# Performance work log

Hardware: AMD Instinct MI355X
Metric: run time of the kernel (lower is better)

The kernel has to match this reference:

```python
import jax, jax.numpy as jnp
import numpy as np

N = 200_000   # nodes per type
F_IN = 64     # input features per node type
H = 8         # hidden_channels (heads=1)
E = 3_000_000 # edges per edge type


def setup_inputs() -> dict:
    key = jax.random.key(0)
    ks = jax.random.split(key, 40)
    d = {}
    d['x_ind'] = jax.random.normal(ks[0], (N, F_IN), jnp.float32)
    d['x_org'] = jax.random.normal(ks[1], (N, F_IN), jnp.float32)
    d['x_ext'] = jax.random.normal(ks[2], (N, F_IN), jnp.float32)
    d['ei_ind_org'] = jax.random.randint(ks[3], (2, E), 0, N, jnp.int32)
    d['ei_org_ind'] = jax.random.randint(ks[4], (2, E), 0, N, jnp.int32)
    d['ei_ext_ind'] = jax.random.randint(ks[5], (2, E), 0, N, jnp.int32)
    d['ei_ext_org'] = jax.random.randint(ks[6], (2, E), 0, N, jnp.int32)
    s_in = 1.0 / np.sqrt(F_IN)
    # per-node-type projections (Linear(F_IN, H) with bias)
    for i, nt in enumerate(('ind', 'org', 'ext')):
        d[f'W_{nt}'] = jax.random.normal(ks[7 + i], (F_IN, H), jnp.float32) * s_in
        d[f'b_{nt}'] = jnp.zeros((H,), jnp.float32)
    # per-edge-type GAT attention vectors (heads=1, so shape [H])
    for i, et in enumerate(('ind_org', 'org_ind', 'ext_ind', 'ext_org')):
        d[f'att_src_{et}'] = jax.random.normal(ks[10 + 2 * i], (H,), jnp.float32) * (1.0 / np.sqrt(H))
        d[f'att_dst_{et}'] = jax.random.normal(ks[11 + 2 * i], (H,), jnp.float32) * (1.0 / np.sqrt(H))
    # semantic attention: k_lin(H->H) + query q
    d['k_W'] = jax.random.normal(ks[20], (H, H), jnp.float32) * (1.0 / np.sqrt(H))
    d['k_b'] = jnp.zeros((H,), jnp.float32)
    d['q'] = jax.random.normal(ks[21], (H,), jnp.float32)
    # prediction heads
    d['lin_ind_W'] = jax.random.normal(ks[22], (H, 1), jnp.float32) * (1.0 / np.sqrt(H))
    d['lin_ind_b'] = jnp.zeros((1,), jnp.float32)
    d['lin_org_W'] = jax.random.normal(ks[23], (H, 1), jnp.float32) * (1.0 / np.sqrt(H))
    d['lin_org_b'] = jnp.zeros((1,), jnp.float32)
    return d


def _gat_edge(h_src, h_dst, a_src, a_dst, ei):
    """Per-edge-type GAT message passing with segment softmax over dst."""
    row, col = ei[0], ei[1]
    alpha_s = h_src @ a_src  # [N]
    alpha_d = h_dst @ a_dst  # [N]
    alpha = jax.nn.leaky_relu(alpha_s[row] + alpha_d[col], 0.2)  # [E]
    m = jax.lax.stop_gradient(jax.ops.segment_max(alpha, col, num_segments=N))
    m = jnp.where(jnp.isfinite(m), m, 0.0)
    ex = jnp.exp(alpha - m[col])
    den = jax.ops.segment_sum(ex, col, num_segments=N) + 1e-16
    w = ex / den[col]  # [E]
    out = jax.ops.segment_sum(h_src[row] * w[:, None], col, num_segments=N)  # [N,H]
    return jax.nn.relu(out)


def _group(outs, q, k_W, k_b):
    """Semantic-level attention over metapath embeddings."""
    o = jnp.stack(outs)  # [M, N, H]
    score = (jnp.tanh(o @ k_W + k_b) @ q).mean(axis=1)  # [M]
    attn = jax.nn.softmax(score)
    return jnp.einsum('m,mnf->nf', attn, o)


def reference(x_ind, x_org, x_ext,
              ei_ind_org, ei_org_ind, ei_ext_ind, ei_ext_org,
              W_ind, b_ind, W_org, b_org, W_ext, b_ext,
              att_src_ind_org, att_dst_ind_org,
              att_src_org_ind, att_dst_org_ind,
              att_src_ext_ind, att_dst_ext_ind,
              att_src_ext_org, att_dst_ext_org,
              k_W, k_b, q,
              lin_ind_W, lin_ind_b, lin_org_W, lin_org_b):
    h_ind = x_ind @ W_ind + b_ind  # [N,H]
    h_org = x_org @ W_org + b_org
    h_ext = x_ext @ W_ext + b_ext
    # metapaths into 'ind'
    outs_ind = [
        _gat_edge(h_org, h_ind, att_src_org_ind, att_dst_org_ind, ei_org_ind),
        _gat_edge(h_ext, h_ind, att_src_ext_ind, att_dst_ext_ind, ei_ext_ind),
    ]
    # metapaths into 'org'
    outs_org = [
        _gat_edge(h_ind, h_org, att_src_ind_org, att_dst_ind_org, ei_ind_org),
        _gat_edge(h_ext, h_org, att_src_ext_org, att_dst_ext_org, ei_ext_org),
    ]
    z_ind = _group(outs_ind, q, k_W, k_b)  # [N,H]
    z_org = _group(outs_org, q, k_W, k_b)
    pred_ind = jax.nn.sigmoid(z_ind @ lin_ind_W + lin_ind_b)[:, 0]
    pred_org = jax.nn.sigmoid(z_org @ lin_org_W + lin_org_b)[:, 0]
    return (pred_ind, pred_org)
```

## Files before the change

kernel.cpp:

```cpp
#include <hip/hip_runtime.h>
#include <hip/hip_fp16.h>

#define HH 8
#define FIN 64
#define CHUNK 8192
#define NPB 1024
#define NPB_SHIFT 10
#define MAXNB 256
#define SUBCH 16384
#define RSH 18
#define RMASK 0x3FFFFu

typedef float vfloat4 __attribute__((ext_vector_type(4)));

__device__ __forceinline__ float b2f(unsigned short u) {
  union { unsigned int i; float f; } x;
  x.i = ((unsigned int)u) << 16;
  return x.f;
}

__device__ __forceinline__ float lrelu(float x) { return x > 0.f ? x : 0.2f * x; }

__device__ __forceinline__ float ld(const void* p, int i, int isf) {
  return isf ? ((const float*)p)[i] : b2f(((const unsigned short*)p)[i]);
}

__device__ __forceinline__ float tanhf_fast(float x) {
  float xc = fminf(fmaxf(x, -15.f), 15.f);
  float e = __expf(2.f * xc);
  return 1.f - 2.f / (e + 1.f);
}

struct MP {
  const int* ei;
  const float* as;
  const float* ad;
  const __half* hs;
  float* den;
  float* out;
  unsigned* sorted;
  int* gcur;
  int E;
  int nchunks;
  int rcap;
};
struct MP4 { MP m[4]; };

struct PJ {
  const void* x; const void* W; const void* b; __half* h16;
  const void* a0; float* s0;
  const void* a1; float* s1;
  const void* a2; float* s2;
};
struct PJ3 { PJ p[3]; };

struct SC { const float *o0, *d0, *o1, *d1; float* score; };
struct SC2 { SC g[2]; };
struct PR { const float *o0, *d0, *o1, *d1; const float* score;
            const void* linW; const void* linb; float* outp; };
struct PR2 { PR g[2]; };

__global__ void __launch_bounds__(1024)
setup_kernel(const unsigned short* __restrict__ x, int* __restrict__ flag,
             float* __restrict__ score_all, int* __restrict__ gcur, int rcap) {
  __shared__ int tot;
  int t = threadIdx.x;
  gcur[t] = (t & 255) * rcap;
  if (t < 4) score_all[t] = 0.f;
  if (t == 0) tot = 0;
  __syncthreads();
  int cnt = 0;
  for (int i = t; i < 2048; i += 1024) {
    int e = (x[i] >> 7) & 0xFF;
    if (e >= 0x90) cnt++;
  }
  if (cnt) atomicAdd(&tot, cnt);
  __syncthreads();
  if (t == 0) flag[0] = (tot >= 8) ? 1 : 0;
}

__global__ void __launch_bounds__(256)
proj_kernel(PJ3 pj, int N, const int* __restrict__ flag) {
  const PJ P = pj.p[blockIdx.y];
  __shared__ float Wl[FIN][HH];
  __shared__ float bl[HH];
  __shared__ float al[3][HH];
  int isf = flag[0];
  int t = threadIdx.x;
  for (int i = t; i < FIN * HH; i += blockDim.x) Wl[i >> 3][i & 7] = ld(P.W, i, isf);
  if (t < HH) {
    bl[t] = ld(P.b, t, isf);
    al[0][t] = P.a0 ? ld(P.a0, t, isf) : 0.f;
    al[1][t] = P.a1 ? ld(P.a1, t, isf) : 0.f;
    al[2][t] = P.a2 ? ld(P.a2, t, isf) : 0.f;
  }
  __syncthreads();
  int n = blockIdx.x * blockDim.x + t;
  if (n >= N) return;
  float acc[HH];
#pragma unroll
  for (int j = 0; j < HH; ++j) acc[j] = bl[j];
  if (isf) {
    const float4* xr = (const float4*)((const float*)P.x + (size_t)n * FIN);
#pragma unroll
    for (int v = 0; v < FIN / 4; ++v) {
      float4 p = xr[v];
      float f4[4] = {p.x, p.y, p.z, p.w};
#pragma unroll
      for (int k = 0; k < 4; ++k) {
        int f = v * 4 + k;
#pragma unroll
        for (int j = 0; j < HH; ++j) acc[j] += f4[k] * Wl[f][j];
      }
    }
  } else {
    const uint4* xr = (const uint4*)((const unsigned short*)P.x + (size_t)n * FIN);
#pragma unroll
    for (int v = 0; v < FIN / 8; ++v) {
      uint4 p = xr[v];
      unsigned int w[4] = {p.x, p.y, p.z, p.w};
#pragma unroll
      for (int k = 0; k < 4; ++k) {
        float f0 = __uint_as_float(w[k] << 16);
        float f1 = __uint_as_float(w[k] & 0xFFFF0000u);
        int f = v * 8 + k * 2;
#pragma unroll
        for (int j = 0; j < HH; ++j) acc[j] += f0 * Wl[f][j];
#pragma unroll
        for (int j = 0; j < HH; ++j) acc[j] += f1 * Wl[f + 1][j];
      }
    }
  }
  union { __half h[8]; uint4 u; } pk;
#pragma unroll
  for (int j = 0; j < HH; ++j) pk.h[j] = __float2half(acc[j]);
  *(uint4*)(P.h16 + (size_t)n * HH) = pk.u;
  float d0 = 0.f, d1 = 0.f, d2 = 0.f;
#pragma unroll
  for (int j = 0; j < HH; ++j) {
    d0 += acc[j] * al[0][j];
    d1 += acc[j] * al[1][j];
    d2 += acc[j] * al[2][j];
  }
  if (P.s0) P.s0[n] = d0;
  if (P.s1) P.s1[n] = d1;
  if (P.s2) P.s2[n] = d2;
}

__global__ void __launch_bounds__(512)
partA(MP4 a4, int mp_base, int NB) {
  const MP a = a4.m[mp_base + blockIdx.y];
  int k = blockIdx.x;
  if (k >= a.nchunks) return;
  __shared__ unsigned buf[CHUNK];
  __shared__ int cnt[MAXNB];
  __shared__ int cur[MAXNB];
  __shared__ int off[MAXNB];
  __shared__ int posA[MAXNB];
  int t = threadIdx.x;
  int E = a.E;
  int base = k * CHUNK;
  int len = E - base; if (len > CHUNK) len = CHUNK;
  if (t < MAXNB) cnt[t] = 0;
  __syncthreads();
  int rr[16], cc[16];
  if (len == CHUNK && ((E & 3) == 0)) {
    const int4* eir = (const int4*)(a.ei + base);
    const int4* eic = (const int4*)(a.ei + E + base);
#pragma unroll
    for (int j = 0; j < 4; ++j) {
      int4 r4 = eir[j * 512 + t];
      int4 c4 = eic[j * 512 + t];
      rr[j * 4 + 0] = r4.x; cc[j * 4 + 0] = c4.x;
      rr[j * 4 + 1] = r4.y; cc[j * 4 + 1] = c4.y;
      rr[j * 4 + 2] = r4.z; cc[j * 4 + 2] = c4.z;
      rr[j * 4 + 3] = r4.w; cc[j * 4 + 3] = c4.w;
    }
  } else {
#pragma unroll
    for (int j = 0; j < 16; ++j) {
      int idx = j * 512 + t;
      rr[j] = -1;
      if (idx < len) { rr[j] = a.ei[base + idx]; cc[j] = a.ei[E + base + idx]; }
    }
  }
#pragma unroll
  for (int j = 0; j < 16; ++j)
    if (rr[j] >= 0) atomicAdd(&cnt[cc[j] >> NPB_SHIFT], 1);
  __syncthreads();
  if (t < 64) {
    int b0 = t * 4;
    int c0 = cnt[b0], c1 = cnt[b0 + 1], c2 = cnt[b0 + 2], c3 = cnt[b0 + 3];
    int s = c0 + c1 + c2 + c3;
    int inc = s;
#pragma unroll
    for (int d = 1; d < 64; d <<= 1) {
      int v = __shfl_up(inc, d, 64);
      if (t >= d) inc += v;
    }
    int run = inc - s;
    off[b0] = run;          cur[b0] = run;
    off[b0 + 1] = run + c0; cur[b0 + 1] = run + c0;
    off[b0 + 2] = run + c0 + c1; cur[b0 + 2] = run + c0 + c1;
    off[b0 + 3] = run + c0 + c1 + c2; cur[b0 + 3] = run + c0 + c1 + c2;
    posA[b0]     = c0 ? atomicAdd(&a.gcur[b0], c0) : 0;
    posA[b0 + 1] = c1 ? atomicAdd(&a.gcur[b0 + 1], c1) : 0;
    posA[b0 + 2] = c2 ? atomicAdd(&a.gcur[b0 + 2], c2) : 0;
    posA[b0 + 3] = c3 ? atomicAdd(&a.gcur[b0 + 3], c3) : 0;
  }
  __syncthreads();
#pragma unroll
  for (int j = 0; j < 16; ++j) {
    if (rr[j] >= 0) {
      int bb = cc[j] >> NPB_SHIFT;
      int p = atomicAdd(&cur[bb], 1);
      buf[p] = ((unsigned)(cc[j] & (NPB - 1)) << RSH) | (unsigned)rr[j];
    }
  }
  __syncthreads();
  int wv = t >> 6, ln = t & 63;
  for (int s = wv; s < NB; s += 8) {
    int cn = cnt[s];
    if (cn == 0) continue;
    int c0 = off[s];
    int gb = posA[s];
    int lim = (s + 1) * a.rcap;
    int mx = lim - gb; if (mx < 0) mx = 0;
    if (cn > mx) cn = mx;
    for (int j = ln; j < cn; j += 64)
      __builtin_nontemporal_store(buf[c0 + j], &a.sorted[(size_t)gb + j]);
  }
}

__global__ void __launch_bounds__(1024)
partB(MP4 a4, int mp_base, int NB, int N, int fused) {
  int mp, b;
  if (fused) {
    int blk = blockIdx.x;
    int xcd = blk & 7;
    mp = xcd >> 1;
    b = ((blk >> 3) << 1) + (xcd & 1);
    if (b >= NB) return;
  } else {
    mp = mp_base;
    b = blockIdx.x;
  }
  const MP a = a4.m[mp];
  __shared__ unsigned key2[SUBCH];
  __shared__ int cnt2[NPB];
  __shared__ int o2[NPB];
  __shared__ int cur2[NPB];
  int t = threadIdx.x;
  int s0i = b * a.rcap;
  int cnt = a.gcur[b] - s0i;
  if (cnt < 0) cnt = 0;
  if (cnt > a.rcap) cnt = a.rcap;
  const unsigned* run = a.sorted + (size_t)s0i;
  int basen = b << NPB_SHIFT;
  int n0 = basen + t;
  float ad0 = (n0 < N) ? a.ad[n0] : 0.f;
  const float* asp = a.as;
  const __half* hs = a.hs;

  float acc0[HH];
#pragma unroll
  for (int f = 0; f < HH; ++f) acc0[f] = 0.f;
  float dn0 = 0.f;

  for (int c0 = 0; c0 < cnt; c0 += SUBCH) {
    int m = cnt - c0; if (m > SUBCH) m = SUBCH;
    cnt2[t] = 0;
    __syncthreads();
    for (int idx = t; idx < m; idx += 1024) {
      unsigned v = __builtin_nontemporal_load(run + c0 + idx);
      atomicAdd(&cnt2[v >> RSH], 1);
    }
    __syncthreads();
    if (t < 64) {
      int c[16];
      int s = 0;
#pragma unroll
      for (int j = 0; j < 16; ++j) { c[j] = cnt2[t * 16 + j]; s += c[j]; }
      int inc = s;
#pragma unroll
      for (int d = 1; d < 64; d <<= 1) {
        int v = __shfl_up(inc, d, 64);
        if (t >= d) inc += v;
      }
      int run2 = inc - s;
#pragma unroll
      for (int j = 0; j < 16; ++j) {
        o2[t * 16 + j] = run2;
        cur2[t * 16 + j] = run2;
        run2 += c[j];
      }
    }
    __syncthreads();
    for (int idx = t; idx < m; idx += 1024) {
      unsigned v = __builtin_nontemporal_load(run + c0 + idx);
      int p = atomicAdd(&cur2[v >> RSH], 1);
      key2[p] = v;
    }
    __syncthreads();
    int j = o2[t], e = cur2[t];
    while (j < e) {
      int cn = e - j; if (cn > 4) cn = 4;
      int r[4];
      float av[4];
      uint4 hv[4];
#pragma unroll
      for (int u = 0; u < 4; ++u) r[u] = (u < cn) ? (int)(key2[j + u] & RMASK) : -1;
#pragma unroll
      for (int u = 0; u < 4; ++u)
        if (r[u] >= 0) { av[u] = asp[r[u]]; hv[u] = *(const uint4*)(hs + (size_t)r[u] * HH); }
#pragma unroll
      for (int u = 0; u < 4; ++u) {
        if (r[u] >= 0) {
          float w = __expf(lrelu(av[u] + ad0));
          dn0 += w;
          union { uint4 q; __half h[8]; } H; H.q = hv[u];
#pragma unroll
          for (int f = 0; f < HH; ++f) acc0[f] += w * __half2float(H.h[f]);
        }
      }
      j += cn;
    }
    if (c0 + SUBCH < cnt) __syncthreads();
  }
  if (n0 < N) {
    vfloat4* po = (vfloat4*)(a.out + (size_t)n0 * HH);
    vfloat4 v0 = {acc0[0], acc0[1], acc0[2], acc0[3]};
    vfloat4 v1 = {acc0[4], acc0[5], acc0[6], acc0[7]};
    __builtin_nontemporal_store(v0, po + 0);
    __builtin_nontemporal_store(v1, po + 1);
    __builtin_nontemporal_store(dn0, &a.den[n0]);
  }
}

__global__ void __launch_bounds__(256)
score_kernel(SC2 sc, int N,
             const void* __restrict__ kW, const void* __restrict__ kb,
             const void* __restrict__ qv, const int* __restrict__ flag) {
  const SC S = sc.g[blockIdx.y];
  __shared__ float kWl[HH][HH];
  __shared__ float kbl[HH], ql[HH];
  __shared__ float r0[4], r1[4];
  int isf = flag[0];
  int t = threadIdx.x;
  if (t < HH * HH) kWl[t >> 3][t & 7] = ld(kW, t, isf);
  if (t < HH) { kbl[t] = ld(kb, t, isf); ql[t] = ld(qv, t, isf); }
  __syncthreads();
  int n = blockIdx.x * blockDim.x + t;
  float s0 = 0.f, s1 = 0.f;
  if (n < N) {
    const float* p0 = S.o0 + (size_t)n * HH;
    const float* p1 = S.o1 + (size_t)n * HH;
    float i0 = 1.f / (S.d0[n] + 1e-16f);
    float i1 = 1.f / (S.d1[n] + 1e-16f);
    float v0[HH], v1[HH];
#pragma unroll
    for (int j = 0; j < HH; ++j) { v0[j] = fmaxf(p0[j] * i0, 0.f); v1[j] = fmaxf(p1[j] * i1, 0.f); }
#pragma unroll
    for (int j = 0; j < HH; ++j) {
      float t0 = kbl[j], t1 = kbl[j];
#pragma unroll
      for (int i = 0; i < HH; ++i) { t0 += v0[i] * kWl[i][j]; t1 += v1[i] * kWl[i][j]; }
      s0 += tanhf_fast(t0) * ql[j];
      s1 += tanhf_fast(t1) * ql[j];
    }
  }
#pragma unroll
  for (int d = 32; d > 0; d >>= 1) {
    s0 += __shfl_down(s0, d, 64);
    s1 += __shfl_down(s1, d, 64);
  }
  int wv = t >> 6, ln = t & 63;
  if (ln == 0) { r0[wv] = s0; r1[wv] = s1; }
  __syncthreads();
  if (t == 0) {
    atomicAdd(&S.score[0], r0[0] + r0[1] + r0[2] + r0[3]);
    atomicAdd(&S.score[1], r1[0] + r1[1] + r1[2] + r1[3]);
  }
}

__global__ void __launch_bounds__(256)
pred_kernel(PR2 pr, int N, const int* __restrict__ flag) {
  const PR P = pr.g[blockIdx.y];
  int isf = flag[0];
  int n = blockIdx.x * blockDim.x + threadIdx.x;
  if (n >= N) return;
  float s0 = P.score[0] / (float)N, s1 = P.score[1] / (float)N;
  float mx = fmaxf(s0, s1);
  float e0 = __expf(s0 - mx), e1 = __expf(s1 - mx);
  float inv = 1.f / (e0 + e1);
  float a0 = e0 * inv, a1 = e1 * inv;
  const float* p0 = P.o0 + (size_t)n * HH;
  const float* p1 = P.o1 + (size_t)n * HH;
  float i0 = 1.f / (P.d0[n] + 1e-16f);
  float i1 = 1.f / (P.d1[n] + 1e-16f);
  float acc = ld(P.linb, 0, isf);
#pragma unroll
  for (int j = 0; j < HH; ++j) {
    float z = a0 * fmaxf(p0[j] * i0, 0.f) + a1 * fmaxf(p1[j] * i1, 0.f);
    acc += z * ld(P.linW, j, isf);
  }
  P.outp[n] = 1.f / (1.f + __expf(-acc));
}

extern "C" void kernel_launch(void* const* d_in, const int* in_sizes, int n_in,
                              void* d_out, int out_size, void* d_ws, size_t ws_size,
                              hipStream_t stream) {
  const int N = in_sizes[0] / FIN;

  const void* x_ind = d_in[0];
  const void* x_org = d_in[1];
  const void* x_ext = d_in[2];
  const int* ei_io = (const int*)d_in[3];  int E_io = in_sizes[3] / 2;
  const int* ei_oi = (const int*)d_in[4];  int E_oi = in_sizes[4] / 2;
  const int* ei_ei = (const int*)d_in[5];  int E_ei = in_sizes[5] / 2;
  const int* ei_eo = (const int*)d_in[6];  int E_eo = in_sizes[6] / 2;
  const void* W_ind = d_in[7];
  const void* b_ind = d_in[8];
  const void* W_org = d_in[9];
  const void* b_org = d_in[10];
  const void* W_ext = d_in[11];
  const void* b_ext = d_in[12];
  const void* att_src_io = d_in[13];
  const void* att_dst_io = d_in[14];
  const void* att_src_oi = d_in[15];
  const void* att_dst_oi = d_in[16];
  const void* att_src_ei = d_in[17];
  const void* att_dst_ei = d_in[18];
  const void* att_src_eo = d_in[19];
  const void* att_dst_eo = d_in[20];
  const void* k_W = d_in[21];
  const void* k_b = d_in[22];
  const void* qv  = d_in[23];
  const void* lin_ind_W = d_in[24];
  const void* lin_ind_b = d_in[25];
  const void* lin_org_W = d_in[26];
  const void* lin_org_b = d_in[27];

  float* out_f = (float*)d_out;

  int E_max = E_io;
  if (E_oi > E_max) E_max = E_oi;
  if (E_ei > E_max) E_max = E_ei;
  if (E_eo > E_max) E_max = E_eo;

  const int NB = (N + NPB - 1) >> NPB_SHIFT;
  const int nchunks_max = (E_max + CHUNK - 1) / CHUNK;
  const int rcap = (int)(((long long)E_max / NB) * 115 / 100) + 128;

  float* ws = (float*)d_ws;
  size_t off = 0;
  __half* h16_ind = (__half*)(ws + off); off += (size_t)N * HH / 2;
  __half* h16_org = (__half*)(ws + off); off += (size_t)N * HH / 2;
  __half* h16_ext = (__half*)(ws + off); off += (size_t)N * HH / 2;
  float* as_io = ws + off; off += N;
  float* ad_oi = ws + off; off += N;
  float* ad_ei = ws + off; off += N;
  float* as_oi = ws + off; off += N;
  float* ad_io = ws + off; off += N;
  float* ad_eo = ws + off; off += N;
  float* as_ei = ws + off; off += N;
  float* as_eo = ws + off; off += N;
  float* den_all = ws + off; off += (size_t)4 * N;
  float* out_all = ws + off; off += (size_t)4 * N * HH;
  float* score_all = ws + off; off += 4;
  int* flag = (int*)(ws + off); off += 1;
  off = (off + 1) & ~(size_t)1;
  int* gcur0 = (int*)(ws + off); off += 4 * 256;

  size_t sort_f = (size_t)NB * rcap;
  bool big = (off + 4 * sort_f) * sizeof(float) <= ws_size;
  int slots = big ? 4 : 1;
  unsigned* sorted0 = (unsigned*)(ws + off); off += (size_t)slots * sort_f;

  const int BS = 256;
  const int nb_node = (N + BS - 1) / BS;

  setup_kernel<<<1, 1024, 0, stream>>>((const unsigned short*)x_ind, flag, score_all, gcur0, rcap);

  PJ3 pj;
  pj.p[0] = PJ{x_ind, W_ind, b_ind, h16_ind, att_src_io, as_io, att_dst_oi, ad_oi, att_dst_ei, ad_ei};
  pj.p[1] = PJ{x_org, W_org, b_org, h16_org, att_src_oi, as_oi, att_dst_io, ad_io, att_dst_eo, ad_eo};
  pj.p[2] = PJ{x_ext, W_ext, b_ext, h16_ext, att_src_ei, as_ei, att_src_eo, as_eo, nullptr, nullptr};
  proj_kernel<<<dim3(nb_node, 3), BS, 0, stream>>>(pj, N, flag);

  const int* eis[4]       = {ei_oi, ei_ei, ei_io, ei_eo};
  int        Es[4]        = {E_oi, E_ei, E_io, E_eo};
  const float* ass[4]     = {as_oi, as_ei, as_io, as_eo};
  const float* ads[4]     = {ad_oi, ad_ei, ad_io, ad_eo};
  const __half* hsrcs[4]  = {h16_org, h16_ext, h16_ind, h16_ext};

  MP4 a4;
  for (int mp = 0; mp < 4; ++mp) {
    MP& a = a4.m[mp];
    a.ei = eis[mp];
    a.as = ass[mp];
    a.ad = ads[mp];
    a.hs = hsrcs[mp];
    a.den = den_all + (size_t)mp * N;
    a.out = out_all + (size_t)mp * N * HH;
    a.sorted = sorted0 + (size_t)(big ? mp : 0) * sort_f;
    a.gcur = gcur0 + mp * 256;
    a.E = Es[mp];
    a.nchunks = (Es[mp] + CHUNK - 1) / CHUNK;
    a.rcap = rcap;
  }

  if (big) {
    partA<<<dim3(nchunks_max, 4), 512, 0, stream>>>(a4, 0, NB);
    int nblkB = 8 * ((NB + 1) >> 1);
    partB<<<dim3(nblkB, 1), 1024, 0, stream>>>(a4, 0, NB, N, 1);
  } else {
    for (int mp = 0; mp < 4; ++mp) {
      partA<<<dim3(a4.m[mp].nchunks, 1), 512, 0, stream>>>(a4, mp, NB);
      partB<<<dim3(NB, 1), 1024, 0, stream>>>(a4, mp, NB, N, 0);
    }
  }

  float* o_ind0 = out_all + (size_t)0 * N * HH;
  float* o_ind1 = out_all + (size_t)1 * N * HH;
  float* o_org0 = out_all + (size_t)2 * N * HH;
  float* o_org1 = out_all + (size_t)3 * N * HH;
  float* d_ind0 = den_all + (size_t)0 * N;
  float* d_ind1 = den_all + (size_t)1 * N;
  float* d_org0 = den_all + (size_t)2 * N;
  float* d_org1 = den_all + (size_t)3 * N;

  SC2 sc;
  sc.g[0] = SC{o_ind0, d_ind0, o_ind1, d_ind1, score_all};
  sc.g[1] = SC{o_org0, d_org0, o_org1, d_org1, score_all + 2};
  score_kernel<<<dim3(nb_node, 2), BS, 0, stream>>>(sc, N, k_W, k_b, qv, flag);

  PR2 pr;
  pr.g[0] = PR{o_ind0, d_ind0, o_ind1, d_ind1, score_all, lin_ind_W, lin_ind_b, out_f};
  pr.g[1] = PR{o_org0, d_org0, o_org1, d_org1, score_all + 2, lin_org_W, lin_org_b, out_f + N};
  pred_kernel<<<dim3(nb_node, 2), BS, 0, stream>>>(pr, N, flag);
}
```

Measured before the change: 591.8 us.

## Pack fp16 features with source attention score into one 32-byte record per metapath

The projection kernel now writes, per metapath, a 32-byte record holding the eight fp16 features and the fp32 source attention logit, replacing separate half-feature and logit arrays. The gather loop in partB then fetches one row per edge instead of two scattered loads. The sort sub-chunk size is halved and the output stores switch from nontemporal to normal stores. The cost is a larger workspace and extra projection writes, since ext features are duplicated into two records.

Result: no change. 599.9 us (+1.4%).

```diff
diff --git a/kernel.cpp b/kernel.cpp
--- a/kernel.cpp
+++ b/kernel.cpp
@@ -7,11 +7,9 @@
 #define NPB 1024
 #define NPB_SHIFT 10
 #define MAXNB 256
-#define SUBCH 16384
+#define SUBCH 8192
 #define RSH 18
 #define RMASK 0x3FFFFu
-
-typedef float vfloat4 __attribute__((ext_vector_type(4)));
 
 __device__ __forceinline__ float b2f(unsigned short u) {
   union { unsigned int i; float f; } x;
@@ -33,9 +31,8 @@
 
 struct MP {
   const int* ei;
-  const float* as;
   const float* ad;
-  const __half* hs;
+  const float* pk;
   float* den;
   float* out;
   unsigned* sorted;
@@ -47,10 +44,11 @@
 struct MP4 { MP m[4]; };
 
 struct PJ {
-  const void* x; const void* W; const void* b; __half* h16;
-  const void* a0; float* s0;
-  const void* a1; float* s1;
-  const void* a2; float* s2;
+  const void* x; const void* W; const void* b;
+  const void* aA; float* pkA;
+  const void* aB; float* pkB;
+  const void* aC; float* sC;
+  const void* aD; float* sD;
 };
 struct PJ3 { PJ p[3]; };
 
@@ -84,15 +82,16 @@
   const PJ P = pj.p[blockIdx.y];
   __shared__ float Wl[FIN][HH];
   __shared__ float bl[HH];
-  __shared__ float al[3][HH];
+  __shared__ float al[4][HH];
   int isf = flag[0];
   int t = threadIdx.x;
   for (int i = t; i < FIN * HH; i += blockDim.x) Wl[i >> 3][i & 7] = ld(P.W, i, isf);
   if (t < HH) {
     bl[t] = ld(P.b, t, isf);
-    al[0][t] = P.a0 ? ld(P.a0, t, isf) : 0.f;
-    al[1][t] = P.a1 ? ld(P.a1, t, isf) : 0.f;
-    al[2][t] = P.a2 ? ld(P.a2, t, isf) : 0.f;
+    al[0][t] = P.aA ? ld(P.aA, t, isf) : 0.f;
+    al[1][t] = P.aB ? ld(P.aB, t, isf) : 0.f;
+    al[2][t] = P.aC ? ld(P.aC, t, isf) : 0.f;
+    al[3][t] = P.aD ? ld(P.aD, t, isf) : 0.f;
   }
   __syncthreads();
   int n = blockIdx.x * blockDim.x + t;
@@ -131,20 +130,29 @@
       }
     }
   }
-  union { __half h[8]; uint4 u; } pk;
-#pragma unroll
-  for (int j = 0; j < HH; ++j) pk.h[j] = __float2half(acc[j]);
-  *(uint4*)(P.h16 + (size_t)n * HH) = pk.u;
-  float d0 = 0.f, d1 = 0.f, d2 = 0.f;
+  union { __half h[8]; uint4 u; } pkh;
+#pragma unroll
+  for (int j = 0; j < HH; ++j) pkh.h[j] = __float2half(acc[j]);
+  float dA = 0.f, dB = 0.f, dC = 0.f, dD = 0.f;
 #pragma unroll
   for (int j = 0; j < HH; ++j) {
-    d0 += acc[j] * al[0][j];
-    d1 += acc[j] * al[1][j];
-    d2 += acc[j] * al[2][j];
-  }
-  if (P.s0) P.s0[n] = d0;
-  if (P.s1) P.s1[n] = d1;
-  if (P.s2) P.s2[n] = d2;
+    dA += acc[j] * al[0][j];
+    dB += acc[j] * al[1][j];
+    dC += acc[j] * al[2][j];
+    dD += acc[j] * al[3][j];
+  }
+  if (P.pkA) {
+    float* rp = P.pkA + (size_t)n * 8;
+    *(uint4*)rp = pkh.u;
+    rp[4] = dA;
+  }
+  if (P.pkB) {
+    float* rp = P.pkB + (size_t)n * 8;
+    *(uint4*)rp = pkh.u;
+    rp[4] = dB;
+  }
+  if (P.sC) P.sC[n] = dC;
+  if (P.sD) P.sD[n] = dD;
 }
 
 __global__ void __launch_bounds__(512)
@@ -259,8 +267,7 @@
   int basen = b << NPB_SHIFT;
   int n0 = basen + t;
   float ad0 = (n0 < N) ? a.ad[n0] : 0.f;
-  const float* asp = a.as;
-  const __half* hs = a.hs;
+  const float* pk = a.pk;
 
   float acc0[HH];
 #pragma unroll
@@ -305,17 +312,22 @@
     int j = o2[t], e = cur2[t];
     while (j < e) {
       int cn = e - j; if (cn > 4) cn = 4;
-      int r[4];
+      int r_[4];
       float av[4];
       uint4 hv[4];
 #pragma unroll
-      for (int u = 0; u < 4; ++u) r[u] = (u < cn) ? (int)(key2[j + u] & RMASK) : -1;
-#pragma unroll
-      for (int u = 0; u < 4; ++u)
-        if (r[u] >= 0) { av[u] = asp[r[u]]; hv[u] = *(const uint4*)(hs + (size_t)r[u] * HH); }
+      for (int u = 0; u < 4; ++u) r_[u] = (u < cn) ? (int)(key2[j + u] & RMASK) : -1;
 #pragma unroll
       for (int u = 0; u < 4; ++u) {
-        if (r[u] >= 0) {
+        if (r_[u] >= 0) {
+          const float* rp = pk + (size_t)r_[u] * 8;
+          hv[u] = *(const uint4*)rp;
+          av[u] = rp[4];
+        }
+      }
+#pragma unroll
+      for (int u = 0; u < 4; ++u) {
+        if (r_[u] >= 0) {
           float w = __expf(lrelu(av[u] + ad0));
           dn0 += w;
           union { uint4 q; __half h[8]; } H; H.q = hv[u];
@@ -328,12 +340,10 @@
     if (c0 + SUBCH < cnt) __syncthreads();
   }
   if (n0 < N) {
-    vfloat4* po = (vfloat4*)(a.out + (size_t)n0 * HH);
-    vfloat4 v0 = {acc0[0], acc0[1], acc0[2], acc0[3]};
-    vfloat4 v1 = {acc0[4], acc0[5], acc0[6], acc0[7]};
-    __builtin_nontemporal_store(v0, po + 0);
-    __builtin_nontemporal_store(v1, po + 1);
-    __builtin_nontemporal_store(dn0, &a.den[n0]);
+    float4* po = (float4*)(a.out + (size_t)n0 * HH);
+    po[0] = make_float4(acc0[0], acc0[1], acc0[2], acc0[3]);
+    po[1] = make_float4(acc0[4], acc0[5], acc0[6], acc0[7]);
+    a.den[n0] = dn0;
   }
 }
 
@@ -454,17 +464,14 @@
 
   float* ws = (float*)d_ws;
   size_t off = 0;
-  __half* h16_ind = (__half*)(ws + off); off += (size_t)N * HH / 2;
-  __half* h16_org = (__half*)(ws + off); off += (size_t)N * HH / 2;
-  __half* h16_ext = (__half*)(ws + off); off += (size_t)N * HH / 2;
-  float* as_io = ws + off; off += N;
+  float* pk0 = ws + off; off += (size_t)N * 8;
+  float* pk1 = ws + off; off += (size_t)N * 8;
+  float* pk2 = ws + off; off += (size_t)N * 8;
+  float* pk3 = ws + off; off += (size_t)N * 8;
   float* ad_oi = ws + off; off += N;
   float* ad_ei = ws + off; off += N;
-  float* as_oi = ws + off; off += N;
   float* ad_io = ws + off; off += N;
   float* ad_eo = ws + off; off += N;
-  float* as_ei = ws + off; off += N;
-  float* as_eo = ws + off; off += N;
   float* den_all = ws + off; off += (size_t)4 * N;
   float* out_all = ws + off; off += (size_t)4 * N * HH;
   float* score_all = ws + off; off += 4;
@@ -483,24 +490,28 @@
   setup_kernel<<<1, 1024, 0, stream>>>((const unsigned short*)x_ind, flag, score_all, gcur0, rcap);
 
   PJ3 pj;
-  pj.p[0] = PJ{x_ind, W_ind, b_ind, h16_ind, att_src_io, as_io, att_dst_oi, ad_oi, att_dst_ei, ad_ei};
-  pj.p[1] = PJ{x_org, W_org, b_org, h16_org, att_src_oi, as_oi, att_dst_io, ad_io, att_dst_eo, ad_eo};
-  pj.p[2] = PJ{x_ext, W_ext, b_ext, h16_ext, att_src_ei, as_ei, att_src_eo, as_eo, nullptr, nullptr};
+  pj.p[0] = PJ{x_ind, W_ind, b_ind,
+               att_src_io, pk2, nullptr, nullptr,
+               att_dst_oi, ad_oi, att_dst_ei, ad_ei};
+  pj.p[1] = PJ{x_org, W_org, b_org,
+               att_src_oi, pk0, nullptr, nullptr,
+               att_dst_io, ad_io, att_dst_eo, ad_eo};
+  pj.p[2] = PJ{x_ext, W_ext, b_ext,
+               att_src_ei, pk1, att_src_eo, pk3,
+               nullptr, nullptr, nullptr, nullptr};
   proj_kernel<<<dim3(nb_node, 3), BS, 0, stream>>>(pj, N, flag);
 
-  const int* eis[4]       = {ei_oi, ei_ei, ei_io, ei_eo};
-  int        Es[4]        = {E_oi, E_ei, E_io, E_eo};
-  const float* ass[4]     = {as_oi, as_ei, as_io, as_eo};
-  const float* ads[4]     = {ad_oi, ad_ei, ad_io, ad_eo};
-  const __half* hsrcs[4]  = {h16_org, h16_ext, h16_ind, h16_ext};
+  const int* eis[4]     = {ei_oi, ei_ei, ei_io, ei_eo};
+  int        Es[4]      = {E_oi, E_ei, E_io, E_eo};
+  const float* ads[4]   = {ad_oi, ad_ei, ad_io, ad_eo};
+  const float* pks[4]   = {pk0, pk1, pk2, pk3};
 
   MP4 a4;
   for (int mp = 0; mp < 4; ++mp) {
     MP& a = a4.m[mp];
     a.ei = eis[mp];
-    a.as = ass[mp];
     a.ad = ads[mp];
-    a.hs = hsrcs[mp];
+    a.pk = pks[mp];
     a.den = den_all + (size_t)mp * N;
     a.out = out_all + (size_t)mp * N * HH;
     a.sorted = sorted0 + (size_t)(big ? mp : 0) * sort_f;
```
